# Performance work log

Measured on AMD Instinct MI355X. Metric: run time of the kernel, lower is better.

## Reference

```python
import jax, jax.numpy as jnp
import numpy as np

N = 1_000_000   # nodes (== number of edges, required by the original code)
E = 1_000_000
NODE_IN, NODE_OUT = 64, 64
EDGE_IN, EDGE_OUT = 16, 64
GRAPH_IN, GRAPH_OUT = 32, 64
ALPHA = 0.2


def setup_inputs() -> dict:
    key = jax.random.key(0)
    ks = jax.random.split(key, 10)
    seg_ids = jnp.sort(jax.random.randint(ks[0], (E,), 0, N, dtype=jnp.int32))
    node_fts = jax.random.normal(ks[1], (N, NODE_IN), dtype=jnp.float32)
    edge_fts = jax.random.normal(ks[2], (E, EDGE_IN), dtype=jnp.float32)
    graph_fts = jax.random.normal(ks[3], (1, GRAPH_IN), dtype=jnp.float32)
    # `edges` is a float matrix whose first column holds the segment ids
    edges = jax.random.normal(ks[4], (E, EDGE_IN), dtype=jnp.float32)
    edges = edges.at[:, 0].set(seg_ids.astype(jnp.float32))
    # parameters (xavier-ish scaled normals)
    def xavier(k, shape, gain=1.0):
        fan_in, fan_out = shape[0], shape[1]
        std = gain * np.sqrt(2.0 / (fan_in + fan_out))
        return jax.random.normal(k, shape, dtype=jnp.float32) * std
    W_node = xavier(ks[5], (NODE_IN, NODE_OUT))
    W_edge = xavier(ks[6], (EDGE_IN, EDGE_OUT))
    W_graph = xavier(ks[7], (GRAPH_IN, GRAPH_OUT))
    a_node = xavier(ks[8], (NODE_OUT + GRAPH_OUT, 1), gain=1.414)
    a_edge = xavier(ks[9], (EDGE_OUT + GRAPH_OUT, 1), gain=1.414)
    return {"node_fts": node_fts, "edge_fts": edge_fts, "graph_fts": graph_fts,
            "edges": edges, "seg_ids": seg_ids, "W_node": W_node,
            "W_edge": W_edge, "W_graph": W_graph, "a_node": a_node,
            "a_edge": a_edge}


def _segment_softmax(att, seg_ids, num_segments):
    # exp(clamp(att)) normalized by per-segment sums, gathered back per row
    att = jnp.exp(jnp.clip(att, -2.0, 2.0))
    sums = jax.ops.segment_sum(att, seg_ids, num_segments=num_segments)
    return att / sums[seg_ids]


def reference(node_fts, edge_fts, graph_fts, edges, seg_ids,
              W_node, W_edge, W_graph, a_node, a_edge):
    h_v = node_fts @ W_node                      # [N, NODE_OUT]
    e_v = edges @ W_edge                         # [E, EDGE_OUT]
    g_v = graph_fts @ W_graph                    # [1, GRAPH_OUT]
    G = g_v.shape[1]
    # concat([g_v.repeat, h_v]) @ a == g_v @ a[:G] + h_v @ a[G:]  (no big concat)
    node_att = jax.nn.leaky_relu(
        (g_v @ a_node[:G] + h_v @ a_node[G:]).squeeze(-1), ALPHA)   # [N]
    edge_att = jax.nn.leaky_relu(
        (g_v @ a_edge[:G] + e_v @ a_edge[G:]).squeeze(-1), ALPHA)   # [E]
    n = node_fts.shape[0]
    node_attention_norm = _segment_softmax(node_att, seg_ids, n)
    edge_attention_norm = _segment_softmax(edge_att, seg_ids, n)
    return (node_attention_norm, edge_attention_norm)
```

## Files before the change

### kernel.cpp

```cpp
#include <hip/hip_runtime.h>

#define ALPHA 0.2f

__global__ void ga_consts_kernel(const float* __restrict__ graph_fts,
                                 const float* __restrict__ W_node,
                                 const float* __restrict__ W_edge,
                                 const float* __restrict__ W_graph,
                                 const float* __restrict__ a_node,
                                 const float* __restrict__ a_edge,
                                 float* __restrict__ consts) {
    const int k = threadIdx.x;

    float g = 0.f;
    #pragma unroll
    for (int c = 0; c < 32; ++c) g += graph_fts[c] * W_graph[c * 64 + k];

    float wn = 0.f;
    #pragma unroll
    for (int c = 0; c < 64; ++c) wn += W_node[k * 64 + c] * a_node[64 + c];
    consts[k] = wn;

    if (k < 16) {
        float we = 0.f;
        #pragma unroll
        for (int c = 0; c < 64; ++c) we += W_edge[k * 64 + c] * a_edge[64 + c];
        consts[64 + k] = we;
    }

    float cn = g * a_node[k];
    float ce = g * a_edge[k];
    #pragma unroll
    for (int off = 32; off > 0; off >>= 1) {
        cn += __shfl_down(cn, off);
        ce += __shfl_down(ce, off);
    }
    if (k == 0) { consts[80] = cn; consts[81] = ce; }
}

__global__ void ga_node_att_kernel(const float* __restrict__ node_fts,
                                   const int* __restrict__ seg_ids,
                                   const float* __restrict__ consts,
                                   float* __restrict__ out_e,
                                   float* __restrict__ sums_node,
                                   int N) {
    const int lane16 = threadIdx.x & 15;
    const int gid = blockIdx.x * blockDim.x + threadIdx.x;
    const int group = gid >> 4;
    const int ngroups = (gridDim.x * blockDim.x) >> 4;

    const float4 w = *reinterpret_cast<const float4*>(&consts[lane16 * 4]);
    const float c_node = consts[80];

    for (int row = group; row < N; row += ngroups) {
        const float4 x = *reinterpret_cast<const float4*>(
            &node_fts[(size_t)row * 64 + lane16 * 4]);
        float d = x.x * w.x + x.y * w.y + x.z * w.z + x.w * w.w;
        d += __shfl_xor(d, 1);
        d += __shfl_xor(d, 2);
        d += __shfl_xor(d, 4);
        d += __shfl_xor(d, 8);
        if (lane16 == 0) {
            float att = c_node + d;
            att = att > 0.f ? att : ALPHA * att;
            att = fminf(fmaxf(att, -2.f), 2.f);
            const float e = expf(att);
            out_e[row] = e;
            atomicAdd(&sums_node[seg_ids[row]], e);
        }
    }
}

__global__ void ga_edge_att_kernel(const float* __restrict__ edges,
                                   const int* __restrict__ seg_ids,
                                   const float* __restrict__ consts,
                                   float* __restrict__ out_e,
                                   float* __restrict__ sums_edge,
                                   int E) {
    const int lane4 = threadIdx.x & 3;
    const int gid = blockIdx.x * blockDim.x + threadIdx.x;
    const int group = gid >> 2;
    const int ngroups = (gridDim.x * blockDim.x) >> 2;

    const float4 w = *reinterpret_cast<const float4*>(&consts[64 + lane4 * 4]);
    const float c_edge = consts[81];

    for (int row = group; row < E; row += ngroups) {
        const float4 x = *reinterpret_cast<const float4*>(
            &edges[(size_t)row * 16 + lane4 * 4]);
        float d = x.x * w.x + x.y * w.y + x.z * w.z + x.w * w.w;
        d += __shfl_xor(d, 1);
        d += __shfl_xor(d, 2);
        if (lane4 == 0) {
            float att = c_edge + d;
            att = att > 0.f ? att : ALPHA * att;
            att = fminf(fmaxf(att, -2.f), 2.f);
            const float e = expf(att);
            out_e[row] = e;
            atomicAdd(&sums_edge[seg_ids[row]], e);
        }
    }
}

__global__ void ga_norm_kernel(const int* __restrict__ seg_ids,
                               const float* __restrict__ sums_node,
                               const float* __restrict__ sums_edge,
                               float* __restrict__ out, int N) {
    int j = blockIdx.x * blockDim.x + threadIdx.x;
    const int stride = gridDim.x * blockDim.x;
    for (; j < N; j += stride) {
        const int s = seg_ids[j];
        out[j]     = out[j]     / sums_node[s];
        out[N + j] = out[N + j] / sums_edge[s];
    }
}

extern "C" void kernel_launch(void* const* d_in, const int* in_sizes, int n_in,
                              void* d_out, int out_size, void* d_ws, size_t ws_size,
                              hipStream_t stream) {
    const float* node_fts  = (const float*)d_in[0];
    const float* graph_fts = (const float*)d_in[2];
    const float* edges     = (const float*)d_in[3];
    const int*   seg_ids   = (const int*)  d_in[4];
    const float* W_node    = (const float*)d_in[5];
    const float* W_edge    = (const float*)d_in[6];
    const float* W_graph   = (const float*)d_in[7];
    const float* a_node    = (const float*)d_in[8];
    const float* a_edge    = (const float*)d_in[9];

    const int N = in_sizes[0] / 64;
    const int E = in_sizes[4];

    float* out       = (float*)d_out;
    float* sums_node = (float*)d_ws;
    float* sums_edge = sums_node + N;
    float* consts    = sums_edge + N;

    hipMemsetAsync(d_ws, 0, (size_t)(2 * N) * sizeof(float), stream);

    ga_consts_kernel<<<1, 64, 0, stream>>>(graph_fts, W_node, W_edge, W_graph,
                                           a_node, a_edge, consts);
    ga_node_att_kernel<<<2048, 256, 0, stream>>>(node_fts, seg_ids, consts,
                                                 out, sums_node, N);
    ga_edge_att_kernel<<<1024, 256, 0, stream>>>(edges, seg_ids, consts,
                                                 out + N, sums_edge, E);
    ga_norm_kernel<<<2048, 256, 0, stream>>>(seg_ids, sums_node, sums_edge, out, N);
}
```

Measured before the change: 441.7 us.

## Widen per-thread loads, drop grid-stride loops, vectorize normalization

The node kernel now uses 4 lanes per row with four float4 loads each instead of 16 lanes with one, and the edge kernel uses one thread per row with a full 64-byte load. All three kernels switch from fixed grid-stride loops to one-pass grids sized to the data. The normalization kernel processes four rows per thread with int4/float4 accesses, and fast __expf replaces expf. The aim is fewer shuffles and more bytes in flight per thread, at the cost of more registers and a slightly less exact exp.

```diff
diff --git a/kernel.cpp b/kernel.cpp
--- a/kernel.cpp
+++ b/kernel.cpp
@@ -37,80 +37,96 @@
     if (k == 0) { consts[80] = cn; consts[81] = ce; }
 }
 
-__global__ void ga_node_att_kernel(const float* __restrict__ node_fts,
-                                   const int* __restrict__ seg_ids,
-                                   const float* __restrict__ consts,
-                                   float* __restrict__ out_e,
-                                   float* __restrict__ sums_node,
-                                   int N) {
-    const int lane16 = threadIdx.x & 15;
+__global__ __launch_bounds__(256)
+void ga_node_att_kernel(const float* __restrict__ node_fts,
+                        const int* __restrict__ seg_ids,
+                        const float* __restrict__ consts,
+                        float* __restrict__ out_e,
+                        float* __restrict__ sums_node,
+                        int N) {
     const int gid = blockIdx.x * blockDim.x + threadIdx.x;
-    const int group = gid >> 4;
-    const int ngroups = (gridDim.x * blockDim.x) >> 4;
+    const int row = gid >> 2;
+    if (row >= N) return;
+    const int lane4 = threadIdx.x & 3;
 
-    const float4 w = *reinterpret_cast<const float4*>(&consts[lane16 * 4]);
-    const float c_node = consts[80];
+    const float4* wp = reinterpret_cast<const float4*>(&consts[lane4 * 16]);
+    const float4 w0 = wp[0], w1 = wp[1], w2 = wp[2], w3 = wp[3];
 
-    for (int row = group; row < N; row += ngroups) {
-        const float4 x = *reinterpret_cast<const float4*>(
-            &node_fts[(size_t)row * 64 + lane16 * 4]);
-        float d = x.x * w.x + x.y * w.y + x.z * w.z + x.w * w.w;
-        d += __shfl_xor(d, 1);
-        d += __shfl_xor(d, 2);
-        d += __shfl_xor(d, 4);
-        d += __shfl_xor(d, 8);
-        if (lane16 == 0) {
-            float att = c_node + d;
-            att = att > 0.f ? att : ALPHA * att;
-            att = fminf(fmaxf(att, -2.f), 2.f);
-            const float e = expf(att);
-            out_e[row] = e;
-            atomicAdd(&sums_node[seg_ids[row]], e);
-        }
+    const float4* xp = reinterpret_cast<const float4*>(
+        &node_fts[(size_t)row * 64 + lane4 * 16]);
+    const float4 x0 = xp[0], x1 = xp[1], x2 = xp[2], x3 = xp[3];
+
+    float d = x0.x * w0.x + x0.y * w0.y + x0.z * w0.z + x0.w * w0.w;
+    d += x1.x * w1.x + x1.y * w1.y + x1.z * w1.z + x1.w * w1.w;
+    d += x2.x * w2.x + x2.y * w2.y + x2.z * w2.z + x2.w * w2.w;
+    d += x3.x * w3.x + x3.y * w3.y + x3.z * w3.z + x3.w * w3.w;
+    d += __shfl_xor(d, 1);
+    d += __shfl_xor(d, 2);
+
+    if (lane4 == 0) {
+        float att = consts[80] + d;
+        att = att > 0.f ? att : ALPHA * att;
+        att = fminf(fmaxf(att, -2.f), 2.f);
+        const float e = __expf(att);
+        out_e[row] = e;
+        atomicAdd(&sums_node[seg_ids[row]], e);
     }
 }
 
-__global__ void ga_edge_att_kernel(const float* __restrict__ edges,
-                                   const int* __restrict__ seg_ids,
-                                   const float* __restrict__ consts,
-                                   float* __restrict__ out_e,
-                                   float* __restrict__ sums_edge,
-                                   int E) {
-    const int lane4 = threadIdx.x & 3;
-    const int gid = blockIdx.x * blockDim.x + threadIdx.x;
-    const int group = gid >> 2;
-    const int ngroups = (gridDim.x * blockDim.x) >> 2;
+__global__ __launch_bounds__(256)
+void ga_edge_att_kernel(const float* __restrict__ edges,
+                        const int* __restrict__ seg_ids,
+                        const float* __restrict__ consts,
+                        float* __restrict__ out_e,
+                        float* __restrict__ sums_edge,
+                        int E) {
+    const int row = blockIdx.x * blockDim.x + threadIdx.x;
+    if (row >= E) return;
 
-    const float4 w = *reinterpret_cast<const float4*>(&consts[64 + lane4 * 4]);
-    const float c_edge = consts[81];
+    const float4* wp = reinterpret_cast<const float4*>(&consts[64]);
+    const float4 w0 = wp[0], w1 = wp[1], w2 = wp[2], w3 = wp[3];
 
-    for (int row = group; row < E; row += ngroups) {
-        const float4 x = *reinterpret_cast<const float4*>(
-            &edges[(size_t)row * 16 + lane4 * 4]);
-        float d = x.x * w.x + x.y * w.y + x.z * w.z + x.w * w.w;
-        d += __shfl_xor(d, 1);
-        d += __shfl_xor(d, 2);
-        if (lane4 == 0) {
-            float att = c_edge + d;
-            att = att > 0.f ? att : ALPHA * att;
-            att = fminf(fmaxf(att, -2.f), 2.f);
-            const float e = expf(att);
-            out_e[row] = e;
-            atomicAdd(&sums_edge[seg_ids[row]], e);
-        }
-    }
+    const float4* xp = reinterpret_cast<const float4*>(&edges[(size_t)row * 16]);
+    const float4 x0 = xp[0], x1 = xp[1], x2 = xp[2], x3 = xp[3];
+
+    float d = x0.x * w0.x + x0.y * w0.y + x0.z * w0.z + x0.w * w0.w;
+    d += x1.x * w1.x + x1.y * w1.y + x1.z * w1.z + x1.w * w1.w;
+    d += x2.x * w2.x + x2.y * w2.y + x2.z * w2.z + x2.w * w2.w;
+    d += x3.x * w3.x + x3.y * w3.y + x3.z * w3.z + x3.w * w3.w;
+
+    float att = consts[81] + d;
+    att = att > 0.f ? att : ALPHA * att;
+    att = fminf(fmaxf(att, -2.f), 2.f);
+    const float e = __expf(att);
+    out_e[row] = e;
+    atomicAdd(&sums_edge[seg_ids[row]], e);
 }
 
-__global__ void ga_norm_kernel(const int* __restrict__ seg_ids,
-                               const float* __restrict__ sums_node,
-                               const float* __restrict__ sums_edge,
-                               float* __restrict__ out, int N) {
-    int j = blockIdx.x * blockDim.x + threadIdx.x;
-    const int stride = gridDim.x * blockDim.x;
-    for (; j < N; j += stride) {
+__global__ __launch_bounds__(256)
+void ga_norm_kernel(const int* __restrict__ seg_ids,
+                    const float* __restrict__ sums_node,
+                    const float* __restrict__ sums_edge,
+                    float* __restrict__ out, int N) {
+    const int q = blockIdx.x * blockDim.x + threadIdx.x;
+    const int n4 = N >> 2;
+    if (q < n4) {
+        float* out2 = out + N;
+        const int4 s = reinterpret_cast<const int4*>(seg_ids)[q];
+        float4 o1 = reinterpret_cast<float4*>(out)[q];
+        float4 o2 = reinterpret_cast<float4*>(out2)[q];
+        o1.x /= sums_node[s.x]; o1.y /= sums_node[s.y];
+        o1.z /= sums_node[s.z]; o1.w /= sums_node[s.w];
+        o2.x /= sums_edge[s.x]; o2.y /= sums_edge[s.y];
+        o2.z /= sums_edge[s.z]; o2.w /= sums_edge[s.w];
+        reinterpret_cast<float4*>(out)[q] = o1;
+        reinterpret_cast<float4*>(out2)[q] = o2;
+    }
+    const int tail_start = n4 << 2;
+    const int j = tail_start + q;
+    if (q < (N - tail_start)) {
         const int s = seg_ids[j];
-        out[j]     = out[j]     / sums_node[s];
-        out[N + j] = out[N + j] / sums_edge[s];
+        out[j]     /= sums_node[s];
+        out[N + j] /= sums_edge[s];
     }
 }
 
@@ -139,9 +155,16 @@
 
     ga_consts_kernel<<<1, 64, 0, stream>>>(graph_fts, W_node, W_edge, W_graph,
                                            a_node, a_edge, consts);
-    ga_node_att_kernel<<<2048, 256, 0, stream>>>(node_fts, seg_ids, consts,
-                                                 out, sums_node, N);
-    ga_edge_att_kernel<<<1024, 256, 0, stream>>>(edges, seg_ids, consts,
-                                                 out + N, sums_edge, E);
-    ga_norm_kernel<<<2048, 256, 0, stream>>>(seg_ids, sums_node, sums_edge, out, N);
+
+    const int node_blocks = (int)(((size_t)N * 4 + 255) / 256);
+    ga_node_att_kernel<<<node_blocks, 256, 0, stream>>>(
+        node_fts, seg_ids, consts, out, sums_node, N);
+
+    const int edge_blocks = (E + 255) / 256;
+    ga_edge_att_kernel<<<edge_blocks, 256, 0, stream>>>(
+        edges, seg_ids, consts, out + N, sums_edge, E);
+
+    const int norm_blocks = ((N >> 2) + 255) / 256;
+    ga_norm_kernel<<<norm_blocks, 256, 0, stream>>>(seg_ids, sums_node,
+                                                    sums_edge, out, N);
 }
```

New measurement: 442.9 us. No clear change (+0.3%).
